# Kernel optimization log

Measured on AMD Instinct MI355X. Metric: run time of the kernel, lower is better.

The kernel has to match this reference:

```python
import jax, jax.numpy as jnp
import numpy as np

SEG_LENS = [2048, 8192]
DIL_RATES = [1, 2]


def _dilated_attention(q, k, v, is_causal):
    # q,k,v: [b, n, h, d]
    b, n, h, d = q.shape
    ng = len(SEG_LENS)
    g = h // ng  # heads per group (even split)
    scale = 1.0 / np.sqrt(d).astype(np.float32)
    out = jnp.zeros_like(q)
    for i, (s, r) in enumerate(zip(SEG_LENS, DIL_RATES)):
        hs = i * g
        offset = i % r  # offset_idx % dilation_rate, as in _create_dilation_pattern
        idx = np.arange(offset, s, r)  # dilated positions within a segment, length m
        m = idx.shape[0]
        ns = n // s  # number of segments
        # reshape to segments then gather dilated positions: [b, ns, m, g, d]
        qg = q[:, :, hs:hs + g, :].reshape(b, ns, s, g, d)[:, :, idx]
        kg = k[:, :, hs:hs + g, :].reshape(b, ns, s, g, d)[:, :, idx]
        vg = v[:, :, hs:hs + g, :].reshape(b, ns, s, g, d)[:, :, idx]
        # segment-local attention over dilated tokens only (structured sparsity)
        scores = jnp.einsum('bsqhd,bskhd->bshqk', qg, kg) * scale
        if is_causal:
            cm = np.tril(np.ones((m, m), dtype=bool))  # idx is sorted -> causal in dilated order
            scores = jnp.where(cm, scores, -jnp.inf)
        attn = jax.nn.softmax(scores, axis=-1)
        og = jnp.einsum('bshqk,bskhd->bsqhd', attn, vg)  # [b, ns, m, g, d]
        # scatter back to full segment positions; non-dilated positions stay zero
        full = jnp.zeros((b, ns, s, g, d), q.dtype).at[:, :, idx].set(og)
        out = out.at[:, :, hs:hs + g, :].set(full.reshape(b, n, g, d))
    return out


def setup_inputs() -> dict:
    key = jax.random.key(0)
    k1, k2, k3 = jax.random.split(key, 3)
    shape = (1, 8192, 8, 64)
    q = jax.random.normal(k1, shape, dtype=jnp.float32)
    k = jax.random.normal(k2, shape, dtype=jnp.float32)
    v = jax.random.normal(k3, shape, dtype=jnp.float32)
    return {"q": q, "k": k, "v": v, "is_causal": 1}


def reference(q, k, v, is_causal):
    return _dilated_attention(q, k, v, bool(is_causal))
```

## Files before the change

### kernel.cpp

```cpp
#include <hip/hip_runtime.h>


#define LP 72

typedef __attribute__((ext_vector_type(8))) short bf16x8;
typedef __attribute__((ext_vector_type(4))) float f32x4;
typedef const unsigned int __attribute__((address_space(1)))* gp1;
typedef unsigned int __attribute__((address_space(3)))* lp3;

__device__ __forceinline__ unsigned short f2bf(float f) {
  unsigned u = __builtin_bit_cast(unsigned, f);
  u += 0x7fff + ((u >> 16) & 1);
  return (unsigned short)(u >> 16);
}

__device__ __forceinline__ int region_base(int head) {
  return (head < 4) ? head * 524288 : 2097152 + (head - 4) * 262144;
}

__device__ __forceinline__ void gl_lds16(const unsigned short* g, unsigned short* l) {
  __builtin_amdgcn_global_load_lds((gp1)g, (lp3)l, 16, 0, 0);
}

__global__ __launch_bounds__(256, 4)
void prep_kernel(const float* __restrict__ K, const float* __restrict__ V,
                 unsigned short* __restrict__ Kb, unsigned short* __restrict__ Vt) {
  __shared__ unsigned short sT[64][LP];
  const int bid = blockIdx.x;
  int head, pos0, rate, off;
  if (bid < 512) { head = bid >> 7; pos0 = (bid & 127) * 64; rate = 1; off = 0; }
  else { int b = bid - 512; head = 4 + (b >> 6); pos0 = (b & 63) * 64; rate = 2; off = 1; }
  const int rb = region_base(head);
  const int tid = threadIdx.x;
  const int row = tid >> 2, dg = tid & 3;
  const long tok = (long)(pos0 + row) * rate + off;

  {
    const float* kp = K + tok * 512 + head * 64 + dg * 16;
    unsigned short tmp[16];
    #pragma unroll
    for (int i = 0; i < 4; ++i) {
      float4 f = ((const float4*)kp)[i];
      tmp[i * 4 + 0] = f2bf(f.x); tmp[i * 4 + 1] = f2bf(f.y);
      tmp[i * 4 + 2] = f2bf(f.z); tmp[i * 4 + 3] = f2bf(f.w);
    }
    const int s = row & 7;
    unsigned short* dstrow = Kb + rb + (long)(pos0 + row) * 64;
    *(int4*)(dstrow + (((2 * dg)     ^ s) * 8)) = ((int4*)tmp)[0];
    *(int4*)(dstrow + (((2 * dg + 1) ^ s) * 8)) = ((int4*)tmp)[1];
  }

  {
    const float* vp = V + tok * 512 + head * 64 + dg * 16;
    #pragma unroll
    for (int i = 0; i < 4; ++i) {
      float4 f = ((const float4*)vp)[i];
      unsigned* p = (unsigned*)&sT[row][dg * 16 + i * 4];
      p[0] = (unsigned)f2bf(f.x) | ((unsigned)f2bf(f.y) << 16);
      p[1] = (unsigned)f2bf(f.z) | ((unsigned)f2bf(f.w) << 16);
    }
  }
  __syncthreads();

  {
    const int wv = tid >> 6, lane = tid & 63;
    unsigned pk[8];
    #pragma unroll
    for (int j = 0; j < 8; ++j) {
      unsigned lo = sT[wv * 16 + 2 * j][lane];
      unsigned hi = sT[wv * 16 + 2 * j + 1][lane];
      pk[j] = lo | (hi << 16);
    }
    const int s = lane & 7;
    unsigned short* dstrow = Vt + rb + (long)pos0 * 64 + lane * 64;
    int4 a = {(int)pk[0], (int)pk[1], (int)pk[2], (int)pk[3]};
    int4 b = {(int)pk[4], (int)pk[5], (int)pk[6], (int)pk[7]};
    *(int4*)(dstrow + (((2 * wv)     ^ s) * 8)) = a;
    *(int4*)(dstrow + (((2 * wv + 1) ^ s) * 8)) = b;
  }
}

__global__ __launch_bounds__(256, 2)
void attn_kernel(const float* __restrict__ Q, const unsigned short* __restrict__ Kb,
                 const unsigned short* __restrict__ Vt, const int* __restrict__ IC,
                 float* __restrict__ O, float* __restrict__ Slots) {
  __shared__ __attribute__((aligned(16))) unsigned short sK[2][4096];
  __shared__ __attribute__((aligned(16))) unsigned short sV[2][4096];
  __shared__ __attribute__((aligned(16))) unsigned short sP[4][1024];

  const int bid = blockIdx.x;
  int head, q0, seg0, mseg, rate, off, grp, chunk, slot;
  if (bid < 512) {
    int h4 = bid & 3;
    int u = bid >> 2;
    chunk = u >> 6;
    int t = 63 - (u & 63);
    head = 4 + h4; seg0 = 0; mseg = 4096;
    rate = 2; off = 1; grp = 1;
    q0 = t * 64;
    slot = (h4 * 64 + t) * 2 + chunk;
  } else {
    int cc = bid - 512;
    int job = (cc & 7) | ((cc >> 8) << 3);
    int tloc = (cc & 255) >> 3;
    head = job & 3;
    seg0 = (job >> 2) * 2048;
    q0 = seg0 + tloc * 64; mseg = 2048;
    rate = 1; off = 0; grp = 0; chunk = 0; slot = 0;
  }
  const int rb = region_base(head);
  const bool causal = (*IC) != 0;
  const int tid = threadIdx.x, wave = tid >> 6, lane = tid & 63;
  const int l16 = lane & 15, quad = lane >> 4;
  const int ch0 = ((quad ^ (l16 & 7)) * 8);
  const int ch1 = ch0 ^ 32;

  const int qloc = q0 - seg0;
  const int diagkb = qloc >> 6;
  const int nkb = causal ? diagkb + 1 : (mseg >> 6);
  const int klo = grp ? chunk * 32 : 0;
  const int khi = grp ? min(nkb, klo + 32) : nkb;
  if (klo >= khi) return;

  const float QSCALE = 0.18033688011112042f;
  bf16x8 aQ[2];
  {
    long tok = (long)(q0 + wave * 16 + l16) * rate + off;
    const float* qp = Q + tok * 512 + head * 64 + quad * 8;
    #pragma unroll
    for (int kc = 0; kc < 2; ++kc) {
      float4 f0 = ((const float4*)(qp + kc * 32))[0];
      float4 f1 = ((const float4*)(qp + kc * 32))[1];
      bf16x8 a;
      a[0] = (short)f2bf(f0.x * QSCALE); a[1] = (short)f2bf(f0.y * QSCALE);
      a[2] = (short)f2bf(f0.z * QSCALE); a[3] = (short)f2bf(f0.w * QSCALE);
      a[4] = (short)f2bf(f1.x * QSCALE); a[5] = (short)f2bf(f1.y * QSCALE);
      a[6] = (short)f2bf(f1.z * QSCALE); a[7] = (short)f2bf(f1.w * QSCALE);
      aQ[kc] = a;
    }
  }

  f32x4 oacc[4], lacc;
  lacc = (f32x4){0.f, 0.f, 0.f, 0.f};
  #pragma unroll
  for (int dt = 0; dt < 4; ++dt) oacc[dt] = (f32x4){0.f, 0.f, 0.f, 0.f};
  bf16x8 vones;
  #pragma unroll
  for (int i = 0; i < 8; ++i) vones[i] = (short)0x3F80;

  unsigned short* myP = &sP[wave][0];
  const unsigned short* Ksrc = Kb + rb + (long)seg0 * 64;
  const unsigned short* Vsrc = Vt + rb + (long)seg0 * 64;

  const int o0 = wave * 1024;
  const int lo = lane * 8;
  {
    const unsigned short* kt = Ksrc + (long)klo * 4096;
    const unsigned short* vt = Vsrc + (long)klo * 4096;
    gl_lds16(kt + o0 + lo,       &sK[0][o0]);
    gl_lds16(kt + o0 + 512 + lo, &sK[0][o0 + 512]);
    gl_lds16(vt + o0 + lo,       &sV[0][o0]);
    gl_lds16(vt + o0 + 512 + lo, &sV[0][o0 + 512]);
  }

  for (int kb = klo; kb < khi; ++kb) {
    const int cur = (kb - klo) & 1;
    __syncthreads();
    if (kb + 1 < khi) {
      const unsigned short* kt = Ksrc + (long)(kb + 1) * 4096;
      const unsigned short* vt = Vsrc + (long)(kb + 1) * 4096;
      gl_lds16(kt + o0 + lo,       &sK[cur ^ 1][o0]);
      gl_lds16(kt + o0 + 512 + lo, &sK[cur ^ 1][o0 + 512]);
      gl_lds16(vt + o0 + lo,       &sV[cur ^ 1][o0]);
      gl_lds16(vt + o0 + 512 + lo, &sV[cur ^ 1][o0 + 512]);
    }
    const unsigned short* kbuf = &sK[cur][0];
    const unsigned short* vbuf = &sV[cur][0];

    f32x4 sc[4];
    #pragma unroll
    for (int c = 0; c < 4; ++c) {
      const unsigned short* krow = &kbuf[(c * 16 + l16) * 64];
      bf16x8 b0 = *(const bf16x8*)(krow + ch0);
      bf16x8 b1 = *(const bf16x8*)(krow + ch1);
      f32x4 z = (f32x4){0.f, 0.f, 0.f, 0.f};
      z = __builtin_amdgcn_mfma_f32_16x16x32_bf16(aQ[0], b0, z, 0, 0, 0);
      z = __builtin_amdgcn_mfma_f32_16x16x32_bf16(aQ[1], b1, z, 0, 0, 0);
      sc[c] = z;
    }

    const bool needMask = causal && (kb == diagkb);
    #pragma unroll
    for (int c = 0; c < 4; ++c) {
      #pragma unroll
      for (int r = 0; r < 4; ++r) {
        float e = __builtin_amdgcn_exp2f(sc[c][r]);
        if (needMask && (kb * 64 + c * 16 + l16 > qloc + wave * 16 + quad * 4 + r)) e = 0.f;
        const int qrow = quad * 4 + r;
        const int cidx = c * 2 + (l16 >> 3);
        myP[qrow * 64 + ((cidx ^ (qrow & 7)) << 3) + (l16 & 7)] = f2bf(e);
      }
    }
    const int swr = l16 & 7;
    bf16x8 aP0 = *(const bf16x8*)&myP[l16 * 64 + ((quad ^ swr) << 3)];
    bf16x8 aP1 = *(const bf16x8*)&myP[l16 * 64 + (((quad + 4) ^ swr) << 3)];
    lacc = __builtin_amdgcn_mfma_f32_16x16x32_bf16(aP0, vones, lacc, 0, 0, 0);
    lacc = __builtin_amdgcn_mfma_f32_16x16x32_bf16(aP1, vones, lacc, 0, 0, 0);

    #pragma unroll
    for (int dt = 0; dt < 4; ++dt) {
      const unsigned short* vrow = &vbuf[(dt * 16 + l16) * 64];
      bf16x8 v0 = *(const bf16x8*)(vrow + ch0);
      bf16x8 v1 = *(const bf16x8*)(vrow + ch1);
      oacc[dt] = __builtin_amdgcn_mfma_f32_16x16x32_bf16(aP0, v0, oacc[dt], 0, 0, 0);
      oacc[dt] = __builtin_amdgcn_mfma_f32_16x16x32_bf16(aP1, v1, oacc[dt], 0, 0, 0);
    }
  }

  if (grp == 1) {
    float* S = Slots + (long)slot * 4160;
    #pragma unroll
    for (int r = 0; r < 4; ++r) {
      int row = wave * 16 + quad * 4 + r;
      #pragma unroll
      for (int dt = 0; dt < 4; ++dt)
        S[row * 64 + dt * 16 + l16] = oacc[dt][r];
    }
    if (l16 == 0) {
      #pragma unroll
      for (int r = 0; r < 4; ++r)
        S[4096 + wave * 16 + quad * 4 + r] = lacc[r];
    }
  } else {
    #pragma unroll
    for (int r = 0; r < 4; ++r) {
      int tq = q0 + wave * 16 + quad * 4 + r;
      long tok = (long)tq * rate + off;
      float inv = 1.0f / lacc[r];
      float* dst = O + tok * 512 + head * 64 + l16;
      #pragma unroll
      for (int dt = 0; dt < 4; ++dt)
        dst[dt * 16] = oacc[dt][r] * inv;
    }
  }
}

__global__ __launch_bounds__(256, 4)
void combine_kernel(const float* __restrict__ Slots, const int* __restrict__ IC,
                    float* __restrict__ O) {
  const int b = blockIdx.x;
  const int h4 = b >> 6, t = b & 63;
  const bool causal = (*IC) != 0;
  const int nkb = causal ? t + 1 : 64;
  const int nc = (nkb > 32) ? 2 : 1;
  const float* s0 = Slots + (long)((h4 * 64 + t) * 2) * 4160;
  const int tid = threadIdx.x;
  const int row = tid >> 2, dq = (tid & 3) * 16;

  float4 acc[4];
  const float4* p0 = (const float4*)(s0 + row * 64 + dq);
  #pragma unroll
  for (int i = 0; i < 4; ++i) acc[i] = p0[i];
  float l = s0[4096 + row];
  if (nc == 2) {
    const float* s1 = s0 + 4160;
    const float4* p1 = (const float4*)(s1 + row * 64 + dq);
    #pragma unroll
    for (int i = 0; i < 4; ++i) {
      float4 v = p1[i];
      acc[i].x += v.x; acc[i].y += v.y; acc[i].z += v.z; acc[i].w += v.w;
    }
    l += s1[4096 + row];
  }
  const float inv = 1.0f / l;
  const long tok = (long)(t * 64 + row) * 2 + 1;
  float* dst = O + tok * 512 + (4 + h4) * 64 + dq;
  #pragma unroll
  for (int i = 0; i < 4; ++i) {
    float4 o = {acc[i].x * inv, acc[i].y * inv, acc[i].z * inv, acc[i].w * inv};
    ((float4*)dst)[i] = o;
  }
  float* dste = O + (tok - 1) * 512 + (4 + h4) * 64 + dq;
  const float4 z = {0.f, 0.f, 0.f, 0.f};
  #pragma unroll
  for (int i = 0; i < 4; ++i) ((float4*)dste)[i] = z;
}

extern "C" void kernel_launch(void* const* d_in, const int* in_sizes, int n_in,
                              void* d_out, int out_size, void* d_ws, size_t ws_size,
                              hipStream_t stream) {
  const float* q = (const float*)d_in[0];
  const float* k = (const float*)d_in[1];
  const float* v = (const float*)d_in[2];
  const int* ic = (const int*)d_in[3];
  unsigned short* Kb = (unsigned short*)d_ws;
  unsigned short* Vt = Kb + 3145728;
  float* Slots = (float*)((char*)d_ws + 12582912);
  prep_kernel<<<dim3(768), dim3(256), 0, stream>>>(k, v, Kb, Vt);
  attn_kernel<<<dim3(1024), dim3(256), 0, stream>>>(q, Kb, Vt, ic, (float*)d_out, Slots);
  combine_kernel<<<dim3(256), dim3(256), 0, stream>>>(Slots, ic, (float*)d_out);
}
```

Before: 138.8 us.

## Split KV range into 16-block chunks for both groups and interleave block scheduling

```diff
diff --git a/kernel.cpp b/kernel.cpp
--- a/kernel.cpp
+++ b/kernel.cpp
@@ -83,30 +83,31 @@
 __global__ __launch_bounds__(256, 2)
 void attn_kernel(const float* __restrict__ Q, const unsigned short* __restrict__ Kb,
                  const unsigned short* __restrict__ Vt, const int* __restrict__ IC,
-                 float* __restrict__ O, float* __restrict__ Slots) {
+                 float* __restrict__ O, float* __restrict__ Slots,
+                 float* __restrict__ Lar) {
   __shared__ __attribute__((aligned(16))) unsigned short sK[2][4096];
   __shared__ __attribute__((aligned(16))) unsigned short sV[2][4096];
   __shared__ __attribute__((aligned(16))) unsigned short sP[4][1024];
 
   const int bid = blockIdx.x;
-  int head, q0, seg0, mseg, rate, off, grp, chunk, slot;
-  if (bid < 512) {
-    int h4 = bid & 3;
-    int u = bid >> 2;
-    chunk = u >> 6;
-    int t = 63 - (u & 63);
-    head = 4 + h4; seg0 = 0; mseg = 4096;
-    rate = 2; off = 1; grp = 1;
-    q0 = t * 64;
-    slot = (h4 * 64 + t) * 2 + chunk;
+  int head, q0, seg0, mseg, rate, off, grp, cnk, tloc, tileId;
+  if ((bid & 1) == 0) {
+    int idx = bid >> 1;
+    tloc = 63 - (idx >> 4);
+    cnk  = (idx >> 2) & 3;
+    int h4 = idx & 3;
+    head = 4 + h4; seg0 = 0; mseg = 4096; rate = 2; off = 1; grp = 1;
+    q0 = tloc * 64;
+    tileId = h4 * 64 + tloc;
   } else {
-    int cc = bid - 512;
-    int job = (cc & 7) | ((cc >> 8) << 3);
-    int tloc = (cc & 255) >> 3;
-    head = job & 3;
-    seg0 = (job >> 2) * 2048;
-    q0 = seg0 + tloc * 64; mseg = 2048;
-    rate = 1; off = 0; grp = 0; chunk = 0; slot = 0;
+    int idx = bid >> 1;
+    tloc = 31 - (idx >> 5);
+    cnk  = (idx >> 4) & 1;
+    int hs = idx & 15;
+    head = hs & 3; seg0 = (hs >> 2) * 2048;
+    mseg = 2048; rate = 1; off = 0; grp = 0;
+    q0 = seg0 + tloc * 64;
+    tileId = 256 + hs * 32 + tloc;
   }
   const int rb = region_base(head);
   const bool causal = (*IC) != 0;
@@ -118,9 +119,10 @@
   const int qloc = q0 - seg0;
   const int diagkb = qloc >> 6;
   const int nkb = causal ? diagkb + 1 : (mseg >> 6);
-  const int klo = grp ? chunk * 32 : 0;
-  const int khi = grp ? min(nkb, klo + 32) : nkb;
+  const int klo = cnk * 16;
+  const int khi = min(nkb, klo + 16);
   if (klo >= khi) return;
+  const int ncnk = (nkb + 15) >> 4;
 
   const float QSCALE = 0.18033688011112042f;
   bf16x8 aQ[2];
@@ -217,21 +219,7 @@
     }
   }
 
-  if (grp == 1) {
-    float* S = Slots + (long)slot * 4160;
-    #pragma unroll
-    for (int r = 0; r < 4; ++r) {
-      int row = wave * 16 + quad * 4 + r;
-      #pragma unroll
-      for (int dt = 0; dt < 4; ++dt)
-        S[row * 64 + dt * 16 + l16] = oacc[dt][r];
-    }
-    if (l16 == 0) {
-      #pragma unroll
-      for (int r = 0; r < 4; ++r)
-        S[4096 + wave * 16 + quad * 4 + r] = lacc[r];
-    }
-  } else {
+  if (ncnk == 1) {
     #pragma unroll
     for (int r = 0; r < 4; ++r) {
       int tq = q0 + wave * 16 + quad * 4 + r;
@@ -241,49 +229,102 @@
       #pragma unroll
       for (int dt = 0; dt < 4; ++dt)
         dst[dt * 16] = oacc[dt][r] * inv;
+      if (grp) {
+        float* dste = O + (tok - 1) * 512 + head * 64 + l16;
+        #pragma unroll
+        for (int dt = 0; dt < 4; ++dt)
+          dste[dt * 16] = 0.f;
+      }
+    }
+  } else if (cnk == 0) {
+    #pragma unroll
+    for (int r = 0; r < 4; ++r) {
+      int tq = q0 + wave * 16 + quad * 4 + r;
+      long tok = (long)tq * rate + off;
+      float* dst = O + tok * 512 + head * 64 + l16;
+      #pragma unroll
+      for (int dt = 0; dt < 4; ++dt)
+        dst[dt * 16] = oacc[dt][r];
+    }
+    if (l16 == 0) {
+      #pragma unroll
+      for (int r = 0; r < 4; ++r)
+        Lar[tileId * 64 + wave * 16 + quad * 4 + r] = lacc[r];
+    }
+  } else {
+    const int slotId = grp ? (tileId * 3 + (cnk - 1)) : (tileId + 512);
+    float* S = Slots + (long)slotId * 4160;
+    #pragma unroll
+    for (int r = 0; r < 4; ++r) {
+      int row = wave * 16 + quad * 4 + r;
+      #pragma unroll
+      for (int dt = 0; dt < 4; ++dt)
+        S[row * 64 + dt * 16 + l16] = oacc[dt][r];
+    }
+    if (l16 == 0) {
+      #pragma unroll
+      for (int r = 0; r < 4; ++r)
+        S[4096 + wave * 16 + quad * 4 + r] = lacc[r];
     }
   }
 }
 
 __global__ __launch_bounds__(256, 4)
-void combine_kernel(const float* __restrict__ Slots, const int* __restrict__ IC,
-                    float* __restrict__ O) {
+void combine_kernel(const float* __restrict__ Slots, const float* __restrict__ Lar,
+                    const int* __restrict__ IC, float* __restrict__ O) {
   const int b = blockIdx.x;
-  const int h4 = b >> 6, t = b & 63;
   const bool causal = (*IC) != 0;
-  const int nkb = causal ? t + 1 : 64;
-  const int nc = (nkb > 32) ? 2 : 1;
-  const float* s0 = Slots + (long)((h4 * 64 + t) * 2) * 4160;
+  int grp, head, tloc, tileId, nkb;
+  int seg0 = 0;
+  if (b < 256) {
+    grp = 1; head = 4 + (b & 3); tloc = b >> 2;
+    tileId = (b & 3) * 64 + tloc;
+    nkb = causal ? tloc + 1 : 64;
+  } else {
+    int u = b - 256;
+    grp = 0; int hs = u & 15; head = hs & 3; seg0 = (hs >> 2) * 2048;
+    tloc = u >> 4;
+    tileId = 256 + hs * 32 + tloc;
+    nkb = causal ? tloc + 1 : 32;
+  }
+  const int ncnk = (nkb + 15) >> 4;
+  if (ncnk < 2) return;
+
   const int tid = threadIdx.x;
   const int row = tid >> 2, dq = (tid & 3) * 16;
+  long tok;
+  if (grp) tok = (long)(tloc * 64 + row) * 2 + 1;
+  else     tok = (long)(seg0 + tloc * 64 + row);
+  float* dst = O + tok * 512 + head * 64 + dq;
 
   float4 acc[4];
-  const float4* p0 = (const float4*)(s0 + row * 64 + dq);
   #pragma unroll
-  for (int i = 0; i < 4; ++i) acc[i] = p0[i];
-  float l = s0[4096 + row];
-  if (nc == 2) {
-    const float* s1 = s0 + 4160;
-    const float4* p1 = (const float4*)(s1 + row * 64 + dq);
+  for (int i = 0; i < 4; ++i) acc[i] = ((const float4*)dst)[i];
+  float l = Lar[tileId * 64 + row];
+
+  for (int c = 1; c < ncnk; ++c) {
+    const int slotId = grp ? (tileId * 3 + (c - 1)) : (tileId + 512);
+    const float* S = Slots + (long)slotId * 4160;
+    const float4* p = (const float4*)(S + row * 64 + dq);
     #pragma unroll
     for (int i = 0; i < 4; ++i) {
-      float4 v = p1[i];
+      float4 v = p[i];
       acc[i].x += v.x; acc[i].y += v.y; acc[i].z += v.z; acc[i].w += v.w;
     }
-    l += s1[4096 + row];
+    l += S[4096 + row];
   }
   const float inv = 1.0f / l;
-  const long tok = (long)(t * 64 + row) * 2 + 1;
-  float* dst = O + tok * 512 + (4 + h4) * 64 + dq;
   #pragma unroll
   for (int i = 0; i < 4; ++i) {
     float4 o = {acc[i].x * inv, acc[i].y * inv, acc[i].z * inv, acc[i].w * inv};
     ((float4*)dst)[i] = o;
   }
-  float* dste = O + (tok - 1) * 512 + (4 + h4) * 64 + dq;
-  const float4 z = {0.f, 0.f, 0.f, 0.f};
-  #pragma unroll
-  for (int i = 0; i < 4; ++i) ((float4*)dste)[i] = z;
+  if (grp) {
+    float* dste = O + (tok - 1) * 512 + head * 64 + dq;
+    const float4 z = {0.f, 0.f, 0.f, 0.f};
+    #pragma unroll
+    for (int i = 0; i < 4; ++i) ((float4*)dste)[i] = z;
+  }
 }
 
 extern "C" void kernel_launch(void* const* d_in, const int* in_sizes, int n_in,
@@ -296,7 +337,8 @@
   unsigned short* Kb = (unsigned short*)d_ws;
   unsigned short* Vt = Kb + 3145728;
   float* Slots = (float*)((char*)d_ws + 12582912);
+  float* Lar = Slots + (long)1280 * 4160;
   prep_kernel<<<dim3(768), dim3(256), 0, stream>>>(k, v, Kb, Vt);
-  attn_kernel<<<dim3(1024), dim3(256), 0, stream>>>(q, Kb, Vt, ic, (float*)d_out, Slots);
-  combine_kernel<<<dim3(256), dim3(256), 0, stream>>>(Slots, ic, (float*)d_out);
-}
+  attn_kernel<<<dim3(2048), dim3(256), 0, stream>>>(q, Kb, Vt, ic, (float*)d_out, Slots, Lar);
+  combine_kernel<<<dim3(768), dim3(256), 0, stream>>>(Slots, Lar, ic, (float*)d_out);
+}
```

After: 156.6 us. +12.8%, slower.

## Keep softmax probabilities in registers via transposed MFMA and permlane swaps

Applied to the files above, without the earlier changes.

```diff
diff --git a/kernel.cpp b/kernel.cpp
--- a/kernel.cpp
+++ b/kernel.cpp
@@ -5,6 +5,7 @@
 
 typedef __attribute__((ext_vector_type(8))) short bf16x8;
 typedef __attribute__((ext_vector_type(4))) float f32x4;
+typedef __attribute__((ext_vector_type(4))) unsigned u32x4;
 typedef const unsigned int __attribute__((address_space(1)))* gp1;
 typedef unsigned int __attribute__((address_space(3)))* lp3;
 
@@ -86,7 +87,6 @@
                  float* __restrict__ O, float* __restrict__ Slots) {
   __shared__ __attribute__((aligned(16))) unsigned short sK[2][4096];
   __shared__ __attribute__((aligned(16))) unsigned short sV[2][4096];
-  __shared__ __attribute__((aligned(16))) unsigned short sP[4][1024];
 
   const int bid = blockIdx.x;
   int head, q0, seg0, mseg, rate, off, grp, chunk, slot;
@@ -140,15 +140,11 @@
     }
   }
 
-  f32x4 oacc[4], lacc;
-  lacc = (f32x4){0.f, 0.f, 0.f, 0.f};
+  f32x4 oacc[4];
+  float lsum = 0.f;
   #pragma unroll
   for (int dt = 0; dt < 4; ++dt) oacc[dt] = (f32x4){0.f, 0.f, 0.f, 0.f};
-  bf16x8 vones;
-  #pragma unroll
-  for (int i = 0; i < 8; ++i) vones[i] = (short)0x3F80;
-
-  unsigned short* myP = &sP[wave][0];
+
   const unsigned short* Ksrc = Kb + rb + (long)seg0 * 64;
   const unsigned short* Vsrc = Vt + rb + (long)seg0 * 64;
 
@@ -162,6 +158,8 @@
     gl_lds16(vt + o0 + lo,       &sV[0][o0]);
     gl_lds16(vt + o0 + 512 + lo, &sV[0][o0 + 512]);
   }
+
+  const int qv = qloc + wave * 16 + l16;
 
   for (int kb = klo; kb < khi; ++kb) {
     const int cur = (kb - klo) & 1;
@@ -184,64 +182,93 @@
       bf16x8 b0 = *(const bf16x8*)(krow + ch0);
       bf16x8 b1 = *(const bf16x8*)(krow + ch1);
       f32x4 z = (f32x4){0.f, 0.f, 0.f, 0.f};
-      z = __builtin_amdgcn_mfma_f32_16x16x32_bf16(aQ[0], b0, z, 0, 0, 0);
-      z = __builtin_amdgcn_mfma_f32_16x16x32_bf16(aQ[1], b1, z, 0, 0, 0);
+      z = __builtin_amdgcn_mfma_f32_16x16x32_bf16(b0, aQ[0], z, 0, 0, 0);
+      z = __builtin_amdgcn_mfma_f32_16x16x32_bf16(b1, aQ[1], z, 0, 0, 0);
       sc[c] = z;
     }
 
-    const bool needMask = causal && (kb == diagkb);
-    #pragma unroll
-    for (int c = 0; c < 4; ++c) {
+    float p[4][4];
+    if (causal && (kb == diagkb)) {
       #pragma unroll
-      for (int r = 0; r < 4; ++r) {
-        float e = __builtin_amdgcn_exp2f(sc[c][r]);
-        if (needMask && (kb * 64 + c * 16 + l16 > qloc + wave * 16 + quad * 4 + r)) e = 0.f;
-        const int qrow = quad * 4 + r;
-        const int cidx = c * 2 + (l16 >> 3);
-        myP[qrow * 64 + ((cidx ^ (qrow & 7)) << 3) + (l16 & 7)] = f2bf(e);
-      }
-    }
-    const int swr = l16 & 7;
-    bf16x8 aP0 = *(const bf16x8*)&myP[l16 * 64 + ((quad ^ swr) << 3)];
-    bf16x8 aP1 = *(const bf16x8*)&myP[l16 * 64 + (((quad + 4) ^ swr) << 3)];
-    lacc = __builtin_amdgcn_mfma_f32_16x16x32_bf16(aP0, vones, lacc, 0, 0, 0);
-    lacc = __builtin_amdgcn_mfma_f32_16x16x32_bf16(aP1, vones, lacc, 0, 0, 0);
+      for (int c = 0; c < 4; ++c)
+        #pragma unroll
+        for (int r = 0; r < 4; ++r) {
+          float e = __builtin_amdgcn_exp2f(sc[c][r]);
+          if (kb * 64 + c * 16 + quad * 4 + r > qv) e = 0.f;
+          p[c][r] = e;
+        }
+    } else {
+      #pragma unroll
+      for (int c = 0; c < 4; ++c)
+        #pragma unroll
+        for (int r = 0; r < 4; ++r)
+          p[c][r] = __builtin_amdgcn_exp2f(sc[c][r]);
+    }
+
+    lsum += (((p[0][0] + p[0][1]) + (p[0][2] + p[0][3])) +
+             ((p[1][0] + p[1][1]) + (p[1][2] + p[1][3]))) +
+            (((p[2][0] + p[2][1]) + (p[2][2] + p[2][3])) +
+             ((p[3][0] + p[3][1]) + (p[3][2] + p[3][3])));
+
+    unsigned W00, W01, W10, W11, W20, W21, W30, W31;
+    asm("v_cvt_pk_bf16_f32 %0, %1, %2" : "=v"(W00) : "v"(p[0][0]), "v"(p[0][1]));
+    asm("v_cvt_pk_bf16_f32 %0, %1, %2" : "=v"(W01) : "v"(p[0][2]), "v"(p[0][3]));
+    asm("v_cvt_pk_bf16_f32 %0, %1, %2" : "=v"(W10) : "v"(p[1][0]), "v"(p[1][1]));
+    asm("v_cvt_pk_bf16_f32 %0, %1, %2" : "=v"(W11) : "v"(p[1][2]), "v"(p[1][3]));
+    asm("v_cvt_pk_bf16_f32 %0, %1, %2" : "=v"(W20) : "v"(p[2][0]), "v"(p[2][1]));
+    asm("v_cvt_pk_bf16_f32 %0, %1, %2" : "=v"(W21) : "v"(p[2][2]), "v"(p[2][3]));
+    asm("v_cvt_pk_bf16_f32 %0, %1, %2" : "=v"(W30) : "v"(p[3][0]), "v"(p[3][1]));
+    asm("v_cvt_pk_bf16_f32 %0, %1, %2" : "=v"(W31) : "v"(p[3][2]), "v"(p[3][3]));
+
+    unsigned R0 = W00, R2 = W10;
+    asm("v_permlane32_swap_b32 %0, %1" : "+v"(R0), "+v"(R2));
+    asm("v_permlane16_swap_b32 %0, %1" : "+v"(R0), "+v"(R2));
+    unsigned R1 = W01, R3 = W11;
+    asm("v_permlane32_swap_b32 %0, %1" : "+v"(R1), "+v"(R3));
+    asm("v_permlane16_swap_b32 %0, %1" : "+v"(R1), "+v"(R3));
+    unsigned R4 = W20, R6 = W30;
+    asm("v_permlane32_swap_b32 %0, %1" : "+v"(R4), "+v"(R6));
+    asm("v_permlane16_swap_b32 %0, %1" : "+v"(R4), "+v"(R6));
+    unsigned R5 = W21, R7 = W31;
+    asm("v_permlane32_swap_b32 %0, %1" : "+v"(R5), "+v"(R7));
+    asm("v_permlane16_swap_b32 %0, %1" : "+v"(R5), "+v"(R7));
+    u32x4 t0 = {R0, R1, R2, R3};
+    u32x4 t1 = {R4, R5, R6, R7};
+    bf16x8 pB0 = __builtin_bit_cast(bf16x8, t0);
+    bf16x8 pB1 = __builtin_bit_cast(bf16x8, t1);
 
     #pragma unroll
     for (int dt = 0; dt < 4; ++dt) {
       const unsigned short* vrow = &vbuf[(dt * 16 + l16) * 64];
       bf16x8 v0 = *(const bf16x8*)(vrow + ch0);
       bf16x8 v1 = *(const bf16x8*)(vrow + ch1);
-      oacc[dt] = __builtin_amdgcn_mfma_f32_16x16x32_bf16(aP0, v0, oacc[dt], 0, 0, 0);
-      oacc[dt] = __builtin_amdgcn_mfma_f32_16x16x32_bf16(aP1, v1, oacc[dt], 0, 0, 0);
-    }
-  }
+      oacc[dt] = __builtin_amdgcn_mfma_f32_16x16x32_bf16(v0, pB0, oacc[dt], 0, 0, 0);
+      oacc[dt] = __builtin_amdgcn_mfma_f32_16x16x32_bf16(v1, pB1, oacc[dt], 0, 0, 0);
+    }
+  }
+
+  float ltot = lsum;
+  ltot += __shfl_xor(ltot, 16);
+  ltot += __shfl_xor(ltot, 32);
 
   if (grp == 1) {
     float* S = Slots + (long)slot * 4160;
-    #pragma unroll
-    for (int r = 0; r < 4; ++r) {
-      int row = wave * 16 + quad * 4 + r;
-      #pragma unroll
-      for (int dt = 0; dt < 4; ++dt)
-        S[row * 64 + dt * 16 + l16] = oacc[dt][r];
-    }
-    if (l16 == 0) {
+    const int qrow = wave * 16 + l16;
+    #pragma unroll
+    for (int dt = 0; dt < 4; ++dt)
       #pragma unroll
       for (int r = 0; r < 4; ++r)
-        S[4096 + wave * 16 + quad * 4 + r] = lacc[r];
-    }
+        S[qrow * 64 + dt * 16 + quad * 4 + r] = oacc[dt][r];
+    if (quad == 0) S[4096 + qrow] = ltot;
   } else {
-    #pragma unroll
-    for (int r = 0; r < 4; ++r) {
-      int tq = q0 + wave * 16 + quad * 4 + r;
-      long tok = (long)tq * rate + off;
-      float inv = 1.0f / lacc[r];
-      float* dst = O + tok * 512 + head * 64 + l16;
+    const int tq = q0 + wave * 16 + l16;
+    const float inv = 1.0f / ltot;
+    float* dst = O + (long)tq * 512 + head * 64 + quad * 4;
+    #pragma unroll
+    for (int dt = 0; dt < 4; ++dt)
       #pragma unroll
-      for (int dt = 0; dt < 4; ++dt)
-        dst[dt * 16] = oacc[dt][r] * inv;
-    }
+      for (int r = 0; r < 4; ++r)
+        dst[dt * 16 + r] = oacc[dt][r] * inv;
   }
 }
 
```

Result: faster. 128.9 us (-7.2%).
